# Kernel tuning notes

Measured on AMD Instinct MI355X. Metric: run time of the kernel, lower is better.

Reference implementation:

```python
import jax, jax.numpy as jnp
import numpy as np

D = 768
HEAD_DIM = 64
NHEADS = D // HEAD_DIM
B, S = 2, 4096


def setup_inputs() -> dict:
    key = jax.random.key(0)
    ks = jax.random.split(key, 9)
    std = 1.0 / np.sqrt(D)
    inp = {"x": jax.random.normal(ks[0], (B, S, D), dtype=jnp.float32)}
    for i, name in enumerate(["Wq", "Wk", "Wv", "Wo"]):
        inp[name + "_w"] = jax.random.uniform(ks[1 + 2 * i], (D, D), dtype=jnp.float32, minval=-std, maxval=std)
        inp[name + "_b"] = jax.random.uniform(ks[2 + 2 * i], (D,), dtype=jnp.float32, minval=-std, maxval=std)
    return inp


def reference(x, Wq_w, Wq_b, Wk_w, Wk_b, Wv_w, Wv_b, Wo_w, Wo_b):
    b, s, d = x.shape
    # nn.Linear: y = x @ W.T + b
    q = x @ Wq_w.T + Wq_b
    k = x @ Wk_w.T + Wk_b
    v = x @ Wv_w.T + Wv_b
    # [B, H, S, hd]
    q = q.reshape(b, s, NHEADS, HEAD_DIM).transpose(0, 2, 1, 3)
    k = k.reshape(b, s, NHEADS, HEAD_DIM).transpose(0, 2, 1, 3)
    v = v.reshape(b, s, NHEADS, HEAD_DIM).transpose(0, 2, 1, 3)
    scale = jnp.sqrt(jnp.asarray(HEAD_DIM, dtype=q.dtype))
    logits = jnp.einsum('bhqd,bhkd->bhqk', q, k) / scale  # [B,H,S,S]
    causal_mask = jnp.triu(jnp.ones((s, s), dtype=bool), k=1)
    logits = jnp.where(causal_mask, -jnp.inf, logits)
    a = jax.nn.softmax(logits, axis=-1)
    preout = jnp.einsum('bhqk,bhkd->bhqd', a, v)
    preout = preout.transpose(0, 2, 1, 3).reshape(b, s, d)
    return preout @ Wo_w.T + Wo_b
```

## Files before the change

### kernel.cpp

```cpp
#include <hip/hip_runtime.h>

typedef unsigned short u16;
typedef unsigned int u32;
typedef __bf16 bf16_t;
typedef bf16_t bf16x8 __attribute__((ext_vector_type(8)));
typedef float f32x4 __attribute__((ext_vector_type(4)));
typedef float f32x16 __attribute__((ext_vector_type(16)));

#define DM 768
#define HD 64
#define NH 12
#define NB 2
#define SEQ 4096
#define MR (NB * SEQ)

#define SCL2E_F (0.125f * 1.44269504088896340736f)

__device__ __forceinline__ u16 f2bf(float f) {
  union { float f; u32 u; } v;
  v.f = f;
  u32 r = v.u + 0x7FFFu + ((v.u >> 16) & 1u);
  return (u16)(r >> 16);
}

__device__ __forceinline__ float fexp2(float x) {
  return __builtin_amdgcn_exp2f(x);
}

__device__ __forceinline__ u32 pk2(float a, float b) {
  union { bf16_t h[2]; u32 u; } x;
  x.h[0] = (bf16_t)a;
  x.h[1] = (bf16_t)b;
  return x.u;
}

__device__ __forceinline__ u32 cvtpk(float a, float b) {
  u32 r;
  asm("v_cvt_pk_bf16_f32 %0, %1, %2" : "=v"(r) : "v"(a), "v"(b));
  return r;
}

__device__ __forceinline__ void pl32swap(u32& a, u32& b) {
  asm volatile("v_permlane32_swap_b32 %0, %1" : "+v"(a), "+v"(b));
}

__device__ __forceinline__ bf16x8 ldb8(const u16* p) {
  return *reinterpret_cast<const bf16x8*>(p);
}

__device__ __forceinline__ f32x4 mfma16(bf16x8 a, bf16x8 b, f32x4 c) {
  return __builtin_amdgcn_mfma_f32_16x16x32_bf16(a, b, c, 0, 0, 0);
}

__device__ __forceinline__ f32x16 mfma32(bf16x8 a, bf16x8 b, f32x16 c) {
  return __builtin_amdgcn_mfma_f32_32x32x16_bf16(a, b, c, 0, 0, 0);
}

#define GLDS16(g, l)                                              \
  __builtin_amdgcn_global_load_lds(                               \
      (const __attribute__((address_space(1))) void*)(g),         \
      (__attribute__((address_space(3))) void*)(l), 16, 0, 0)

__global__ __launch_bounds__(256) void cvt_kernel(const float* __restrict__ src,
                                                  u16* __restrict__ dst, int n8) {
  int i = blockIdx.x * 256 + threadIdx.x;
  if (i >= n8) return;
  const float4* s = reinterpret_cast<const float4*>(src) + (size_t)i * 2;
  float4 a = s[0], b = s[1];
  union { u16 u[8]; uint4 v; } o;
  o.u[0] = f2bf(a.x); o.u[1] = f2bf(a.y); o.u[2] = f2bf(a.z); o.u[3] = f2bf(a.w);
  o.u[4] = f2bf(b.x); o.u[5] = f2bf(b.y); o.u[6] = f2bf(b.z); o.u[7] = f2bf(b.w);
  reinterpret_cast<uint4*>(dst)[i] = o.v;
}

__global__ __launch_bounds__(256) void cvt_w_kernel(const float* __restrict__ w0,
                                                    const float* __restrict__ w1,
                                                    const float* __restrict__ w2,
                                                    const float* __restrict__ w3,
                                                    u16* __restrict__ dst) {
  const float* src = (blockIdx.y == 0) ? w0 : (blockIdx.y == 1) ? w1
                   : (blockIdx.y == 2) ? w2 : w3;
  u16* d = dst + (size_t)blockIdx.y * DM * DM;
  int i = blockIdx.x * 256 + threadIdx.x;
  const float4* s = reinterpret_cast<const float4*>(src) + (size_t)i * 2;
  float4 a = s[0], b = s[1];
  union { u16 u[8]; uint4 v; } o;
  o.u[0] = f2bf(a.x); o.u[1] = f2bf(a.y); o.u[2] = f2bf(a.z); o.u[3] = f2bf(a.w);
  o.u[4] = f2bf(b.x); o.u[5] = f2bf(b.y); o.u[6] = f2bf(b.z); o.u[7] = f2bf(b.w);
  reinterpret_cast<uint4*>(d)[i] = o.v;
}

__global__ __launch_bounds__(256) void gemm_qkv_kernel(
    const u16* __restrict__ A, const u16* __restrict__ Wall,
    const float* __restrict__ b0, const float* __restrict__ b1,
    const float* __restrict__ b2, u16* __restrict__ O) {
  __shared__ __align__(16) u16 As[128 * 32];
  __shared__ __align__(16) u16 Bs[128 * 32];

  const int tid = threadIdx.x;
  const int w = tid >> 6, lane = tid & 63;
  const int l16 = lane & 15, lg = lane >> 4;
  const int wm = w >> 1, wn = w & 1;

  const int m0 = blockIdx.x * 128;
  const int n0 = blockIdx.y * 128;
  const int z = blockIdx.z;

  const u16* W = Wall + (size_t)z * DM * DM;
  const float* bias = (z == 0) ? b0 : ((z == 1) ? b1 : b2);
  u16* oz = O + (size_t)z * MR * DM;
  const float qscale = (z == 0) ? SCL2E_F : 1.f;

  f32x4 acc[4][4];
#pragma unroll
  for (int i = 0; i < 4; ++i)
#pragma unroll
    for (int j = 0; j < 4; ++j) {
      acc[i][j][0] = 0.f; acc[i][j][1] = 0.f;
      acc[i][j][2] = 0.f; acc[i][j][3] = 0.f;
    }

  for (int k0 = 0; k0 < DM; k0 += 32) {
#pragma unroll
    for (int i = 0; i < 2; ++i) {
      const int c = (w * 2 + i) * 64 + lane;
      const int m = c >> 2, kc = c & 3;
      GLDS16(A + (size_t)(m0 + m) * DM + (k0 + kc * 8),
             As + (size_t)(w * 2 + i) * 512);
      GLDS16(W + (size_t)(n0 + m) * DM + (k0 + kc * 8),
             Bs + (size_t)(w * 2 + i) * 512);
    }
    __syncthreads();
    bf16x8 af[4], bfv[4];
#pragma unroll
    for (int i = 0; i < 4; ++i)
      af[i] = ldb8(As + (wm * 64 + i * 16 + l16) * 32 + lg * 8);
#pragma unroll
    for (int j = 0; j < 4; ++j)
      bfv[j] = ldb8(Bs + (wn * 64 + j * 16 + l16) * 32 + lg * 8);
#pragma unroll
    for (int i = 0; i < 4; ++i)
#pragma unroll
      for (int j = 0; j < 4; ++j)
        acc[i][j] = mfma16(af[i], bfv[j], acc[i][j]);
    __syncthreads();
  }

#pragma unroll
  for (int i = 0; i < 4; ++i) {
    const int gm = m0 + wm * 64 + i * 16 + lg * 4;
    const int bb = gm >> 12;
    const int ss = gm & (SEQ - 1);
#pragma unroll
    for (int j = 0; j < 4; ++j) {
      const int gn = n0 + wn * 64 + j * 16 + l16;
      const int hh = gn >> 6, dd = gn & (HD - 1);
      const float bv = bias[gn];
      if (z == 2) {
        union { u16 u[4]; uint2 v; } pk;
#pragma unroll
        for (int r = 0; r < 4; ++r) pk.u[r] = f2bf(acc[i][j][r] + bv);
        *reinterpret_cast<uint2*>(
            oz + ((size_t)(bb * NH + hh) * HD + dd) * SEQ + ss) = pk.v;
      } else {
        u16* op = oz + ((size_t)(bb * NH + hh) * SEQ + ss) * HD + dd;
#pragma unroll
        for (int r = 0; r < 4; ++r)
          op[(size_t)r * HD] = f2bf((acc[i][j][r] + bv) * qscale);
      }
    }
  }
}

__global__ __launch_bounds__(256) void gemm_out_kernel(
    const u16* __restrict__ A, const u16* __restrict__ W,
    const float* __restrict__ bias, float* __restrict__ Out) {
  __shared__ __align__(16) u16 As[128 * 32];
  __shared__ __align__(16) u16 Bs[128 * 32];

  const int tid = threadIdx.x;
  const int w = tid >> 6, lane = tid & 63;
  const int l16 = lane & 15, lg = lane >> 4;
  const int wm = w >> 1, wn = w & 1;

  const int m0 = blockIdx.x * 128;
  const int n0 = blockIdx.y * 128;

  f32x4 acc[4][4];
#pragma unroll
  for (int i = 0; i < 4; ++i)
#pragma unroll
    for (int j = 0; j < 4; ++j) {
      acc[i][j][0] = 0.f; acc[i][j][1] = 0.f;
      acc[i][j][2] = 0.f; acc[i][j][3] = 0.f;
    }

  for (int k0 = 0; k0 < DM; k0 += 32) {
#pragma unroll
    for (int i = 0; i < 2; ++i) {
      const int c = (w * 2 + i) * 64 + lane;
      const int m = c >> 2, kc = c & 3;
      GLDS16(A + (size_t)(m0 + m) * DM + (k0 + kc * 8),
             As + (size_t)(w * 2 + i) * 512);
      GLDS16(W + (size_t)(n0 + m) * DM + (k0 + kc * 8),
             Bs + (size_t)(w * 2 + i) * 512);
    }
    __syncthreads();
    bf16x8 af[4], bfv[4];
#pragma unroll
    for (int i = 0; i < 4; ++i)
      af[i] = ldb8(As + (wm * 64 + i * 16 + l16) * 32 + lg * 8);
#pragma unroll
    for (int j = 0; j < 4; ++j)
      bfv[j] = ldb8(Bs + (wn * 64 + j * 16 + l16) * 32 + lg * 8);
#pragma unroll
    for (int i = 0; i < 4; ++i)
#pragma unroll
      for (int j = 0; j < 4; ++j)
        acc[i][j] = mfma16(af[i], bfv[j], acc[i][j]);
    __syncthreads();
  }

#pragma unroll
  for (int i = 0; i < 4; ++i) {
    const int gm = m0 + wm * 64 + i * 16 + lg * 4;
#pragma unroll
    for (int j = 0; j < 4; ++j) {
      const int gn = n0 + wn * 64 + j * 16 + l16;
      const float bv = bias[gn];
      float* op = Out + (size_t)gm * DM + gn;
#pragma unroll
      for (int r = 0; r < 4; ++r)
        op[(size_t)r * DM] = acc[i][j][r] + bv;
    }
  }
}

__global__ __launch_bounds__(256) void attn_kernel(
    const u16* __restrict__ Qg, const u16* __restrict__ Kg,
    const u16* __restrict__ VTg, u16* __restrict__ Og) {
  __shared__ __align__(16) u16 Kt[2][64 * 64];
  __shared__ __align__(16) u16 Vt[2][64 * 64];

  const int tid = threadIdx.x;
  const int w = tid >> 6, lane = tid & 63;
  const int l32 = lane & 31, hi = lane >> 5;

  const int idx = blockIdx.x;
  const int x8 = idx & 7;
  const int g = idx >> 3;
  const int qt = 31 - g / 3;
  const int bh = (g % 3) * 8 + x8;
  const int bb = bh / NH, hh = bh % NH;

  const u16* Qp = Qg + (size_t)bh * SEQ * HD;
  const u16* Kp = Kg + (size_t)bh * SEQ * HD;
  const u16* VTp = VTg + (size_t)bh * HD * SEQ;

  const int qw0 = qt * 128 + w * 32;
  const int qlane = qw0 + l32;

  bf16x8 qf[4];
#pragma unroll
  for (int c = 0; c < 4; ++c)
    qf[c] = ldb8(Qp + (size_t)qlane * HD + c * 16 + hi * 8);

  f32x16 oacc[2];
  f32x16 zero16;
#pragma unroll
  for (int r = 0; r < 16; ++r) zero16[r] = 0.f;
#pragma unroll
  for (int db = 0; db < 2; ++db)
#pragma unroll
    for (int r = 0; r < 16; ++r) oacc[db][r] = 0.f;
  float lsum = 0.f;

  const int srow = tid >> 3;
  const int sc8 = (tid & 7) * 8;
  const int sww = (srow & 7) << 3;
  const int wi0 = (srow * 64 + sc8) ^ sww;
  const int wi1 = ((srow + 32) * 64 + sc8) ^ sww;
  const int swr = (l32 & 7) << 3;

  const u16* kP0 = Kp + (size_t)srow * HD + sc8;
  const u16* kP1 = kP0 + (size_t)32 * HD;
  const u16* vP0 = VTp + (size_t)srow * SEQ + sc8;
  const u16* vP1 = vP0 + (size_t)32 * SEQ;

  {
    uint4 a = *reinterpret_cast<const uint4*>(kP0);
    uint4 b = *reinterpret_cast<const uint4*>(kP1);
    uint4 c = *reinterpret_cast<const uint4*>(vP0);
    uint4 d = *reinterpret_cast<const uint4*>(vP1);
    *reinterpret_cast<uint4*>(&Kt[0][wi0]) = a;
    *reinterpret_cast<uint4*>(&Kt[0][wi1]) = b;
    *reinterpret_cast<uint4*>(&Vt[0][wi0]) = c;
    *reinterpret_cast<uint4*>(&Vt[0][wi1]) = d;
  }
  kP0 += (size_t)64 * HD; kP1 += (size_t)64 * HD;
  vP0 += 64; vP1 += 64;

  const int NT = 2 * qt + 2;
  int cur = 0;
  for (int t = 0; t < NT; ++t) {
    const int kv0 = t * 64;
    const bool pf = (t + 1 < NT);
    uint4 nK0, nK1, nV0, nV1;
    if (pf) {
      nK0 = *reinterpret_cast<const uint4*>(kP0);
      nK1 = *reinterpret_cast<const uint4*>(kP1);
      nV0 = *reinterpret_cast<const uint4*>(vP0);
      nV1 = *reinterpret_cast<const uint4*>(vP1);
    }
    kP0 += (size_t)64 * HD; kP1 += (size_t)64 * HD;
    vP0 += 64; vP1 += 64;
    __syncthreads();

    const bool active = (kv0 <= qw0 + 31);
    f32x16 st[2];
    if (active) {
      __builtin_amdgcn_s_setprio(1);
#pragma unroll
      for (int b = 0; b < 2; ++b) {
        {
          bf16x8 kf = ldb8(&Kt[cur][((b * 32 + l32) * 64 + (hi * 8)) ^ swr]);
          st[b] = mfma32(kf, qf[0], zero16);
        }
#pragma unroll
        for (int c = 1; c < 4; ++c) {
          bf16x8 kf = ldb8(
              &Kt[cur][((b * 32 + l32) * 64 + (c * 16 + hi * 8)) ^ swr]);
          st[b] = mfma32(kf, qf[c], st[b]);
        }
      }
      __builtin_amdgcn_s_setprio(0);

      if (kv0 + 63 > qw0) {
#pragma unroll
        for (int b = 0; b < 2; ++b)
#pragma unroll
          for (int r = 0; r < 16; ++r) {
            const int kvi = kv0 + b * 32 + (r & 3) + 8 * (r >> 2) + 4 * hi;
            if (kvi > qlane) st[b][r] = -__builtin_inff();
          }
      }

#pragma unroll
      for (int r = 0; r < 16; ++r) {
        st[0][r] = fexp2(st[0][r]);
        st[1][r] = fexp2(st[1][r]);
      }
      {
        float sm[8];
#pragma unroll
        for (int r = 0; r < 8; ++r)
          sm[r] = (st[0][r] + st[0][r + 8]) + (st[1][r] + st[1][r + 8]);
#pragma unroll
        for (int r = 0; r < 4; ++r) sm[r] += sm[r + 4];
        lsum += (sm[0] + sm[2]) + (sm[1] + sm[3]);
      }
    }

    if (pf) {
      *reinterpret_cast<uint4*>(&Kt[cur ^ 1][wi0]) = nK0;
      *reinterpret_cast<uint4*>(&Kt[cur ^ 1][wi1]) = nK1;
      *reinterpret_cast<uint4*>(&Vt[cur ^ 1][wi0]) = nV0;
      *reinterpret_cast<uint4*>(&Vt[cur ^ 1][wi1]) = nV1;
    }

    if (active) {
#pragma unroll
      for (int b = 0; b < 2; ++b) {
#pragma unroll
        for (int h = 0; h < 2; ++h) {
          u32 a0 = pk2(st[b][h * 8 + 0], st[b][h * 8 + 1]);
          u32 a1 = pk2(st[b][h * 8 + 2], st[b][h * 8 + 3]);
          u32 a2 = pk2(st[b][h * 8 + 4], st[b][h * 8 + 5]);
          u32 a3 = pk2(st[b][h * 8 + 6], st[b][h * 8 + 7]);
          pl32swap(a0, a2);
          pl32swap(a1, a3);
          union { u32 w[4]; bf16x8 v; } pb;
          pb.w[0] = a0; pb.w[1] = a1; pb.w[2] = a2; pb.w[3] = a3;
          const int c = 2 * b + h;
          __builtin_amdgcn_s_setprio(1);
#pragma unroll
          for (int db = 0; db < 2; ++db) {
            bf16x8 vf = ldb8(
                &Vt[cur][((db * 32 + l32) * 64 + (c * 16 + hi * 8)) ^ swr]);
            oacc[db] = mfma32(vf, pb.v, oacc[db]);
          }
          __builtin_amdgcn_s_setprio(0);
        }
      }
    }
    cur ^= 1;
  }

  const float ltot = lsum + __shfl_xor(lsum, 32);
  const float linv = 1.f / ltot;

  u16* Op = Og + ((size_t)bb * SEQ + qlane) * DM + hh * HD;
#pragma unroll
  for (int db = 0; db < 2; ++db)
#pragma unroll
    for (int r = 0; r < 16; r += 2) {
      const int d = db * 32 + (r & 3) + 8 * (r >> 2) + 4 * hi;
      u32 pk = cvtpk(oacc[db][r] * linv, oacc[db][r + 1] * linv);
      *reinterpret_cast<u32*>(Op + d) = pk;
    }
}

extern "C" void kernel_launch(void* const* d_in, const int* in_sizes, int n_in,
                              void* d_out, int out_size, void* d_ws,
                              size_t ws_size, hipStream_t stream) {
  const float* x  = (const float*)d_in[0];
  const float* Wq = (const float*)d_in[1];
  const float* bq = (const float*)d_in[2];
  const float* Wk = (const float*)d_in[3];
  const float* bk = (const float*)d_in[4];
  const float* Wv = (const float*)d_in[5];
  const float* bv = (const float*)d_in[6];
  const float* Wo = (const float*)d_in[7];
  const float* bo = (const float*)d_in[8];
  float* out = (float*)d_out;

  u16* xb   = (u16*)d_ws;
  u16* Wall = xb + (size_t)MR * DM;
  u16* QKV  = Wall + (size_t)4 * DM * DM;
  u16* PRE  = QKV + (size_t)3 * MR * DM;

  cvt_kernel<<<dim3(MR * DM / 8 / 256), 256, 0, stream>>>(x, xb, MR * DM / 8);
  cvt_w_kernel<<<dim3(DM * DM / 8 / 256, 4), 256, 0, stream>>>(Wq, Wk, Wv, Wo,
                                                               Wall);
  gemm_qkv_kernel<<<dim3(MR / 128, DM / 128, 3), 256, 0, stream>>>(
      xb, Wall, bq, bk, bv, QKV);
  attn_kernel<<<dim3(768), 256, 0, stream>>>(
      QKV, QKV + (size_t)MR * DM, QKV + (size_t)2 * MR * DM, PRE);
  gemm_out_kernel<<<dim3(MR / 128, DM / 128), 256, 0, stream>>>(
      PRE, Wall + (size_t)3 * DM * DM, bo, out);
}
```

Before: 173.7 us.

## Split long causal query tiles across two blocks and combine partials

The attention grid becomes 1152 blocks. Query tiles 16-31 have their KV range split into two halves handled by separate blocks, and a longest-first schedule table orders the work. The split halves write unnormalized bf16 partial outputs and row sums to workspace (reusing the xb region). A new combine kernel adds the halves and normalizes them. This is meant to fix load imbalance and tail effects from causal work growing with tile index. It costs an extra launch, extra memory traffic and a bf16 rounding of the partials. It relies on the running max being fixed (no max rescaling) so that partials can simply be added.

```diff
diff --git a/kernel.cpp b/kernel.cpp
--- a/kernel.cpp
+++ b/kernel.cpp
@@ -48,6 +48,12 @@
   return *reinterpret_cast<const bf16x8*>(p);
 }
 
+__device__ __forceinline__ float bf2f(u16 u) {
+  union { u32 u; float f; } v;
+  v.u = (u32)u << 16;
+  return v.f;
+}
+
 __device__ __forceinline__ f32x4 mfma16(bf16x8 a, bf16x8 b, f32x4 c) {
   return __builtin_amdgcn_mfma_f32_16x16x32_bf16(a, b, c, 0, 0, 0);
 }
@@ -60,6 +66,11 @@
   __builtin_amdgcn_global_load_lds(                               \
       (const __attribute__((address_space(1))) void*)(g),         \
       (__attribute__((address_space(3))) void*)(l), 16, 0, 0)
+
+__device__ __constant__ unsigned char kOrder[48] = {
+    15, 46, 47, 44, 45, 14, 42, 43, 40, 41, 13, 38, 39, 36, 37, 12,
+    34, 35, 32, 33, 11, 30, 31, 28, 29, 10, 26, 27, 24, 25, 9,  22,
+    23, 20, 21, 8,  18, 19, 16, 17, 7,  6,  5,  4,  3,  2,  1,  0};
 
 __global__ __launch_bounds__(256) void cvt_kernel(const float* __restrict__ src,
                                                   u16* __restrict__ dst, int n8) {
@@ -238,7 +249,8 @@
 
 __global__ __launch_bounds__(256) void attn_kernel(
     const u16* __restrict__ Qg, const u16* __restrict__ Kg,
-    const u16* __restrict__ VTg, u16* __restrict__ Og) {
+    const u16* __restrict__ VTg, u16* __restrict__ Og,
+    u16* __restrict__ PO, float* __restrict__ PL) {
   __shared__ __align__(16) u16 Kt[2][64 * 64];
   __shared__ __align__(16) u16 Vt[2][64 * 64];
 
@@ -248,9 +260,21 @@
 
   const int idx = blockIdx.x;
   const int x8 = idx & 7;
-  const int g = idx >> 3;
-  const int qt = 31 - g / 3;
-  const int bh = (g % 3) * 8 + x8;
+  const int gg = idx >> 3;
+  const int bh = (gg % 3) * 8 + x8;
+  const int rank = gg / 3;
+  const int j = kOrder[rank];
+  int qt, t0, t1, half = 0;
+  bool direct;
+  if (j < 16) {
+    qt = j; t0 = 0; t1 = 2 * j + 2; direct = true;
+  } else {
+    const int s = j - 16;
+    qt = 16 + (s >> 1);
+    half = s & 1;
+    const int L = qt + 1;
+    t0 = half * L; t1 = t0 + L; direct = false;
+  }
   const int bb = bh / NH, hh = bh % NH;
 
   const u16* Qp = Qg + (size_t)bh * SEQ * HD;
@@ -282,9 +306,9 @@
   const int wi1 = ((srow + 32) * 64 + sc8) ^ sww;
   const int swr = (l32 & 7) << 3;
 
-  const u16* kP0 = Kp + (size_t)srow * HD + sc8;
+  const u16* kP0 = Kp + (size_t)(t0 * 64 + srow) * HD + sc8;
   const u16* kP1 = kP0 + (size_t)32 * HD;
-  const u16* vP0 = VTp + (size_t)srow * SEQ + sc8;
+  const u16* vP0 = VTp + (size_t)srow * SEQ + t0 * 64 + sc8;
   const u16* vP1 = vP0 + (size_t)32 * SEQ;
 
   {
@@ -300,11 +324,10 @@
   kP0 += (size_t)64 * HD; kP1 += (size_t)64 * HD;
   vP0 += 64; vP1 += 64;
 
-  const int NT = 2 * qt + 2;
   int cur = 0;
-  for (int t = 0; t < NT; ++t) {
+  for (int t = t0; t < t1; ++t) {
     const int kv0 = t * 64;
-    const bool pf = (t + 1 < NT);
+    const bool pf = (t + 1 < t1);
     uint4 nK0, nK1, nV0, nV1;
     if (pf) {
       nK0 = *reinterpret_cast<const uint4*>(kP0);
@@ -397,17 +420,66 @@
   }
 
   const float ltot = lsum + __shfl_xor(lsum, 32);
-  const float linv = 1.f / ltot;
-
-  u16* Op = Og + ((size_t)bb * SEQ + qlane) * DM + hh * HD;
-#pragma unroll
-  for (int db = 0; db < 2; ++db)
-#pragma unroll
-    for (int r = 0; r < 16; r += 2) {
-      const int d = db * 32 + (r & 3) + 8 * (r >> 2) + 4 * hi;
-      u32 pk = cvtpk(oacc[db][r] * linv, oacc[db][r + 1] * linv);
-      *reinterpret_cast<u32*>(Op + d) = pk;
-    }
+  const int qrow = w * 32 + l32;
+
+  if (direct) {
+    const float linv = 1.f / ltot;
+    u16* Op = Og + ((size_t)bb * SEQ + qlane) * DM + hh * HD;
+#pragma unroll
+    for (int db = 0; db < 2; ++db)
+#pragma unroll
+      for (int r = 0; r < 16; r += 2) {
+        const int d = db * 32 + (r & 3) + 8 * (r >> 2) + 4 * hi;
+        u32 pk = cvtpk(oacc[db][r] * linv, oacc[db][r + 1] * linv);
+        *reinterpret_cast<u32*>(Op + d) = pk;
+      }
+  } else {
+    const int grp = bh * 16 + (qt - 16);
+    u16* pbase = PO + (((size_t)grp * 2 + half) * 128 + qrow) * 64;
+#pragma unroll
+    for (int db = 0; db < 2; ++db)
+#pragma unroll
+      for (int r = 0; r < 16; r += 2) {
+        const int d = db * 32 + (r & 3) + 8 * (r >> 2) + 4 * hi;
+        u32 pk = cvtpk(oacc[db][r], oacc[db][r + 1]);
+        *reinterpret_cast<u32*>(pbase + d) = pk;
+      }
+    if (hi == 0) PL[((size_t)grp * 2 + half) * 128 + qrow] = ltot;
+  }
+}
+
+__global__ __launch_bounds__(256) void combine_kernel(
+    const u16* __restrict__ PO, const float* __restrict__ PL,
+    u16* __restrict__ Og) {
+  const int grp = blockIdx.x;
+  const int bh = grp >> 4, qt16 = grp & 15;
+  const int bb = bh / NH, hh = bh % NH;
+  const int tid = threadIdx.x;
+  const int q = tid >> 1;
+  const int d0 = (tid & 1) * 32;
+  const u16* p0 = PO + (((size_t)grp * 2 + 0) * 128 + q) * 64 + d0;
+  const u16* p1 = PO + (((size_t)grp * 2 + 1) * 128 + q) * 64 + d0;
+  const float linv =
+      1.f / (PL[((size_t)grp * 2 + 0) * 128 + q] +
+             PL[((size_t)grp * 2 + 1) * 128 + q]);
+  union { uint4 v[4]; u16 u[32]; } a0, a1;
+#pragma unroll
+  for (int i = 0; i < 4; ++i) {
+    a0.v[i] = reinterpret_cast<const uint4*>(p0)[i];
+    a1.v[i] = reinterpret_cast<const uint4*>(p1)[i];
+  }
+  const int srow = (16 + qt16) * 128 + q;
+  u16* op = Og + ((size_t)bb * SEQ + srow) * DM + hh * HD + d0;
+  u32 pk[16];
+#pragma unroll
+  for (int i = 0; i < 16; ++i) {
+    const float e0 = (bf2f(a0.u[2 * i]) + bf2f(a1.u[2 * i])) * linv;
+    const float e1 = (bf2f(a0.u[2 * i + 1]) + bf2f(a1.u[2 * i + 1])) * linv;
+    pk[i] = cvtpk(e0, e1);
+  }
+#pragma unroll
+  for (int i = 0; i < 4; ++i)
+    reinterpret_cast<uint4*>(op)[i] = *reinterpret_cast<const uint4*>(&pk[4 * i]);
 }
 
 extern "C" void kernel_launch(void* const* d_in, const int* in_sizes, int n_in,
@@ -428,14 +500,17 @@
   u16* Wall = xb + (size_t)MR * DM;
   u16* QKV  = Wall + (size_t)4 * DM * DM;
   u16* PRE  = QKV + (size_t)3 * MR * DM;
+  u16* PO   = (u16*)d_ws;
+  float* PL = (float*)(PRE + (size_t)MR * DM);
 
   cvt_kernel<<<dim3(MR * DM / 8 / 256), 256, 0, stream>>>(x, xb, MR * DM / 8);
   cvt_w_kernel<<<dim3(DM * DM / 8 / 256, 4), 256, 0, stream>>>(Wq, Wk, Wv, Wo,
                                                                Wall);
   gemm_qkv_kernel<<<dim3(MR / 128, DM / 128, 3), 256, 0, stream>>>(
       xb, Wall, bq, bk, bv, QKV);
-  attn_kernel<<<dim3(768), 256, 0, stream>>>(
-      QKV, QKV + (size_t)MR * DM, QKV + (size_t)2 * MR * DM, PRE);
+  attn_kernel<<<dim3(1152), 256, 0, stream>>>(
+      QKV, QKV + (size_t)MR * DM, QKV + (size_t)2 * MR * DM, PRE, PO, PL);
+  combine_kernel<<<dim3(384), 256, 0, stream>>>(PO, PL, PRE);
   gemm_out_kernel<<<dim3(MR / 128, DM / 128), 256, 0, stream>>>(
       PRE, Wall + (size_t)3 * DM * DM, bo, out);
 }
```

Result: slower. 185.2 us (+6.6%).
